# Kernel optimization log

Hardware: AMD Instinct MI355X
Metric: run time of the kernel (lower is better)

The kernel has to match this reference:

```python
import jax, jax.numpy as jnp
import numpy as np
import math

PATCH = 41
NUM_ANG = 8
NUM_SPATIAL = 4
BIN_KSIZE = 2 * int(PATCH / (NUM_SPATIAL + 1))   # 16
BIN_STRIDE = PATCH // NUM_SPATIAL                # 10
BIN_PAD = BIN_KSIZE // 4                         # 4
CLIPVAL = 0.2
EPS = 1e-10
N = 8192


def _sift_pooling_kernel(ksize: int) -> np.ndarray:
    k2 = float(ksize) / 2.0
    xc2 = k2 - np.abs(np.arange(ksize, dtype=np.float32) + 0.5 - k2)
    return (np.outer(xc2, xc2) / k2 ** 2).astype(np.float32)


def _sift_weighting_kernel(ksize: int) -> np.ndarray:
    # Gauss, vlfeat sigma: sigma_mul_2 = ksize**2
    k2 = float(ksize) / 2.0
    ys = np.arange(ksize, dtype=np.float32)[:, None]
    xs = np.arange(ksize, dtype=np.float32)[None, :]
    disq = (ys - k2 + 0.5) ** 2 + (xs - k2 + 0.5) ** 2
    return np.exp(-disq / float(ksize ** 2)).astype(np.float32)


def setup_inputs() -> dict:
    key = jax.random.key(0)
    x = jax.random.normal(key, (N, 1, PATCH, PATCH), dtype=jnp.float32)
    gk = jnp.asarray(_sift_weighting_kernel(PATCH))   # [41,41]
    pk = jnp.asarray(_sift_pooling_kernel(BIN_KSIZE))  # [16,16]
    return {"x": x, "gk": gk, "pk": pk}


def _l2_normalize(v):
    return v / jnp.maximum(jnp.linalg.norm(v, axis=1, keepdims=True), 1e-12)


def reference(x, gk, pk):
    # gradients via replicate-pad + central difference (matches [-1,0,1] convs)
    xp = jnp.pad(x, ((0, 0), (0, 0), (0, 0), (1, 1)), mode='edge')
    gx = xp[..., 2:] - xp[..., :-2]
    yp = jnp.pad(x, ((0, 0), (0, 0), (1, 1), (0, 0)), mode='edge')
    gy = yp[:, :, 2:, :] - yp[:, :, :-2, :]

    mag = jnp.sqrt(gx * gx + gy * gy + EPS) * gk  # gaussian-weighted magnitude
    ori = jnp.arctan2(gy, gx + EPS)

    # soft angular binning
    o_big = (ori + 2.0 * math.pi) / (2.0 * math.pi) * NUM_ANG
    bo0f = jnp.floor(o_big)
    wo1 = o_big - bo0f
    bo0 = bo0f.astype(jnp.int32) % NUM_ANG
    bo1 = (bo0 + 1) % NUM_ANG
    # [N,1,P,P,nb]
    contrib = (jax.nn.one_hot(bo0, NUM_ANG, dtype=mag.dtype) * ((1.0 - wo1) * mag)[..., None]
               + jax.nn.one_hot(bo1, NUM_ANG, dtype=mag.dtype) * (wo1 * mag)[..., None])
    contrib = jnp.transpose(contrib[:, 0], (0, 3, 1, 2))  # [N,nb,P,P]

    # depthwise weighted spatial pooling (same triangular kernel per angular bin)
    kern = jnp.broadcast_to(pk[None, None], (NUM_ANG, 1, BIN_KSIZE, BIN_KSIZE))
    pooled = jax.lax.conv_general_dilated(
        contrib, kern,
        window_strides=(BIN_STRIDE, BIN_STRIDE),
        padding=[(BIN_PAD, BIN_PAD), (BIN_PAD, BIN_PAD)],
        feature_group_count=NUM_ANG,
        dimension_numbers=('NCHW', 'OIHW', 'NCHW'))  # [N,nb,4,4]

    desc = pooled.reshape(pooled.shape[0], -1)  # [N,128]
    desc = _l2_normalize(desc)
    desc = jnp.clip(desc, 0.0, CLIPVAL)
    desc = _l2_normalize(desc)
    # rootsift: sqrt of L1-normalized descriptor
    desc = desc / jnp.maximum(jnp.sum(jnp.abs(desc), axis=1, keepdims=True), 1e-12)
    return jnp.sqrt(desc + 1e-10)
```

## Files before the change

### kernel.cpp

```cpp
#include <hip/hip_runtime.h>
#include <hip/hip_fp16.h>
#include <math.h>

#define PATCH 41
#define PP 1681
#define NB 8
#define STRIDE 10
#define PAD 4
#define NTH 192
#define XR 51
#define HR 5

__device__ __forceinline__ constexpr float tri16(int k) {
    float d = (float)k + 0.5f - 8.0f;
    float a = d < 0.0f ? -d : d;
    return (8.0f - a) * 0.125f;
}

__device__ __forceinline__ uint4 pixel_contrib(float gx, float gy, float w) {
    float X = gx + 1e-10f;
    float mag = __builtin_amdgcn_sqrtf(fmaf(gx, gx, fmaf(gy, gy, 1e-10f))) * w;

    float ax = fabsf(X), ay = fabsf(gy);
    float mx = fmaxf(ax, ay), mn = fminf(ax, ay);
    float r = mn * __builtin_amdgcn_rcpf(fmaxf(mx, 1e-30f));
    float r2 = r * r;
    float a4 = fmaf(r2, -0.0149238f, 0.0670406f);
    a4 = fmaf(r2, a4, -0.1482457f);
    a4 = fmaf(r2, a4, 0.2464287f);
    a4 = fmaf(r2, a4, -0.4235106f);
    a4 = fmaf(r2, a4, 1.2732106f);
    a4 *= r;

    bool sw = ay > ax;
    bool xn = X < 0.0f;
    bool yn = gy < 0.0f;
    int q = (xn ? 2 : 0) + ((sw != xn) ? 1 : 0);
    int b0 = yn ? 7 - q : q;
    bool f = (sw != xn) != yn;
    float ma = a4 * mag;
    float mb = mag - ma;
    float v0 = f ? ma : mb;
    float v1 = f ? mb : ma;

    unsigned combo = __builtin_bit_cast(unsigned, __builtin_amdgcn_cvt_pkrtz(v0, v1));
    int sh = (b0 & 3) << 4;
    unsigned long long A = (unsigned long long)combo << sh;
    unsigned long long B = ((b0 & 3) == 3) ? (unsigned long long)(combo >> 16) : 0ull;
    bool lohalf = b0 < 4;
    unsigned long long lo = lohalf ? A : B;
    unsigned long long hi = lohalf ? B : A;
    uint4 cw;
    cw.x = (unsigned)lo; cw.y = (unsigned)(lo >> 32);
    cw.z = (unsigned)hi; cw.w = (unsigned)(hi >> 32);
    return cw;
}

__global__ __launch_bounds__(NTH, 8) void sift_desc_kernel(
        const float* __restrict__ x,
        const float* __restrict__ gk,
        const float* __restrict__ pk,
        float* __restrict__ out)
{
    const int patch = blockIdx.x;
    const int t = threadIdx.x;

    __shared__ __align__(16) float s_xp[PATCH * XR];
    __shared__ __align__(16) float s_wl[64];
    __shared__ __align__(16) __half s_H[49 * HR * NB];
    __shared__ float s_desc[128];

    const float* xp = x + (size_t)patch * PP;
    {
        int i = t / PATCH;
        int j = t - i * PATCH;
        for (int p = t; p < PP; p += NTH) {
            s_xp[i * XR + j + 6] = xp[p];
            j += 28; i += 4;
            if (j >= PATCH) { j -= PATCH; i += 1; }
        }
    }
    for (int q = t; q < 41 * 9; q += NTH) {
        int i = q / 9;
        int c = q - i * 9;
        int j = (c < 6) ? (c - 6) : (c + 35);
        int jc = min(max(j, 0), PATCH - 1);
        s_xp[i * XR + j + 6] = xp[i * PATCH + jc];
    }
    if (t < 64) {
        int ox = t >> 4, kx = t & 15;
        int col = ox * STRIDE - PAD + kx;
        float d = (float)(col - 20);
        float g = __builtin_amdgcn_exp2f(d * d * -8.582362e-4f);
        bool oob = (col < 0) | (col > PATCH - 1);
        s_wl[t] = oob ? 0.0f : tri16(kx) * g;
    }
    if (t < 160) {
        int dw = (t < 80) ? t : (820 + t);
        ((unsigned*)s_H)[dw] = 0u;
    }
    __syncthreads();

    if (t < PATCH * 4) {
        const int row = t >> 2;
        const int ox = t & 3;
        const int rowM = row * XR + ox * STRIDE + 2;
        const int rowU = (row > 0 ? row - 1 : 0) * XR + ox * STRIDE + 2;
        const int rowD = (row < PATCH - 1 ? row + 1 : PATCH - 1) * XR + ox * STRIDE + 2;

        float drow = (float)(row - 20);
        const float rf = __builtin_amdgcn_exp2f(drow * drow * -8.582362e-4f);

        float wf[16];
        {
            const float4* wl4 = (const float4*)&s_wl[ox << 4];
            float4 w0 = wl4[0], w1 = wl4[1], w2 = wl4[2], w3 = wl4[3];
            wf[0] = w0.x * rf;  wf[1] = w0.y * rf;  wf[2] = w0.z * rf;  wf[3] = w0.w * rf;
            wf[4] = w1.x * rf;  wf[5] = w1.y * rf;  wf[6] = w1.z * rf;  wf[7] = w1.w * rf;
            wf[8] = w2.x * rf;  wf[9] = w2.y * rf;  wf[10] = w2.z * rf; wf[11] = w2.w * rf;
            wf[12] = w3.x * rf; wf[13] = w3.y * rf; wf[14] = w3.z * rf; wf[15] = w3.w * rf;
        }

        float xm1 = s_xp[rowM - 1];
        float x0  = s_xp[rowM];
        float x1  = s_xp[rowM + 1];

        const __half2 z2 = __float2half2_rn(0.0f);
        __half2 a0 = z2, a1 = z2, a2 = z2, a3 = z2;

        #pragma unroll
        for (int it = 0; it < 8; ++it) {
            const int kx0 = 2 * it;
            float x2 = s_xp[rowM + kx0 + 2];
            float x3 = s_xp[rowM + kx0 + 3];
            float u0 = s_xp[rowU + kx0];
            float u1 = s_xp[rowU + kx0 + 1];
            float d0 = s_xp[rowD + kx0];
            float d1 = s_xp[rowD + kx0 + 1];

            uint4 c0 = pixel_contrib(x1 - xm1, d0 - u0, wf[kx0]);
            uint4 c1 = pixel_contrib(x2 - x0,  d1 - u1, wf[kx0 + 1]);

            a0 = __hadd2(a0, __hadd2(*(__half2*)&c0.x, *(__half2*)&c1.x));
            a1 = __hadd2(a1, __hadd2(*(__half2*)&c0.y, *(__half2*)&c1.y));
            a2 = __hadd2(a2, __hadd2(*(__half2*)&c0.z, *(__half2*)&c1.z));
            a3 = __hadd2(a3, __hadd2(*(__half2*)&c0.w, *(__half2*)&c1.w));

            xm1 = x1; x0 = x2; x1 = x3;
        }

        uint4 hv;
        hv.x = *(unsigned*)&a0;
        hv.y = *(unsigned*)&a1;
        hv.z = *(unsigned*)&a2;
        hv.w = *(unsigned*)&a3;
        *(uint4*)&s_H[((row + 4) * HR + ox) * NB] = hv;
    }
    __syncthreads();

    if (t < 128) {
        int b = t >> 4;
        int oy = (t >> 2) & 3;
        int ox = t & 3;
        const __half* hp = &s_H[(oy * STRIDE * HR + ox) * NB + b];
        float v = 0.0f;
        #pragma unroll
        for (int ky = 0; ky < 16; ++ky) {
            v = fmaf(tri16(ky), __half2float(hp[ky * HR * NB]), v);
        }
        s_desc[t] = v;
    }
    __syncthreads();

    if (t < 64) {
        float a = s_desc[t];
        float b = s_desc[t + 64];

        float ss = fmaf(a, a, b * b);
        #pragma unroll
        for (int o = 32; o > 0; o >>= 1) ss += __shfl_xor(ss, o);
        float inv = 1.0f / fmaxf(__builtin_amdgcn_sqrtf(ss), 1e-12f);
        a = fminf(fmaxf(a * inv, 0.0f), 0.2f);
        b = fminf(fmaxf(b * inv, 0.0f), 0.2f);

        float ss2 = fmaf(a, a, b * b);
        #pragma unroll
        for (int o = 32; o > 0; o >>= 1) ss2 += __shfl_xor(ss2, o);
        float inv2 = 1.0f / fmaxf(__builtin_amdgcn_sqrtf(ss2), 1e-12f);
        a *= inv2; b *= inv2;

        float l1 = a + b;
        #pragma unroll
        for (int o = 32; o > 0; o >>= 1) l1 += __shfl_xor(l1, o);
        float invl = 1.0f / fmaxf(l1, 1e-12f);

        float* op = out + (size_t)patch * 128;
        op[t]      = __builtin_amdgcn_sqrtf(fmaf(a, invl, 1e-10f));
        op[t + 64] = __builtin_amdgcn_sqrtf(fmaf(b, invl, 1e-10f));
    }
}

extern "C" void kernel_launch(void* const* d_in, const int* in_sizes, int n_in,
                              void* d_out, int out_size, void* d_ws, size_t ws_size,
                              hipStream_t stream) {
    const float* x  = (const float*)d_in[0];
    const float* gk = (const float*)d_in[1];
    const float* pk = (const float*)d_in[2];
    float* out = (float*)d_out;
    const int n = in_sizes[0] / PP;
    sift_desc_kernel<<<n, NTH, 0, stream>>>(x, gk, pk, out);
}
```

Baseline: 117.1 us.

## Share overlapping horizontal pixel contributions across lanes via DPP instead of recomputing

Each thread now evaluates pixel_contrib for only 11 unique columns of its row segment instead of the full 16-wide pooling window. The overlapping columns owned by neighbouring column threads are pulled in with DPP row shifts and weighted by the triangular kernel in fp16 FMA. This removes the duplicated gradient, orientation and magnitude work caused by the overlapping 16-wide, stride-10 windows. In exchange it adds cross-lane DPP operations and edge masking, and moves the triangular weighting into fp16 arithmetic, which can change rounding.

Result: no change. 115.4 us (-1.5%).

```diff
diff --git a/kernel.cpp b/kernel.cpp
--- a/kernel.cpp
+++ b/kernel.cpp
@@ -56,6 +56,17 @@
     return cw;
 }
 
+__device__ __forceinline__ __half2 u2h2(unsigned v) {
+    return __builtin_bit_cast(__half2, v);
+}
+
+__device__ __forceinline__ unsigned dpp_prev(unsigned v) {
+    return (unsigned)__builtin_amdgcn_update_dpp(0, (int)v, 0x111, 0xF, 0xF, true);
+}
+__device__ __forceinline__ unsigned dpp_next(unsigned v) {
+    return (unsigned)__builtin_amdgcn_update_dpp(0, (int)v, 0x101, 0xF, 0xF, true);
+}
+
 __global__ __launch_bounds__(NTH, 8) void sift_desc_kernel(
         const float* __restrict__ x,
         const float* __restrict__ gk,
@@ -66,7 +77,7 @@
     const int t = threadIdx.x;
 
     __shared__ __align__(16) float s_xp[PATCH * XR];
-    __shared__ __align__(16) float s_wl[64];
+    __shared__ __align__(16) float s_gc[48];
     __shared__ __align__(16) __half s_H[49 * HR * NB];
     __shared__ float s_desc[128];
 
@@ -87,13 +98,10 @@
         int jc = min(max(j, 0), PATCH - 1);
         s_xp[i * XR + j + 6] = xp[i * PATCH + jc];
     }
-    if (t < 64) {
-        int ox = t >> 4, kx = t & 15;
-        int col = ox * STRIDE - PAD + kx;
-        float d = (float)(col - 20);
+    if (t < 48) {
+        float d = (float)(t - 20);
         float g = __builtin_amdgcn_exp2f(d * d * -8.582362e-4f);
-        bool oob = (col < 0) | (col > PATCH - 1);
-        s_wl[t] = oob ? 0.0f : tri16(kx) * g;
+        s_gc[t] = (t < PATCH) ? g : 0.0f;
     }
     if (t < 160) {
         int dw = (t < 80) ? t : (820 + t);
@@ -104,22 +112,13 @@
     if (t < PATCH * 4) {
         const int row = t >> 2;
         const int ox = t & 3;
-        const int rowM = row * XR + ox * STRIDE + 2;
-        const int rowU = (row > 0 ? row - 1 : 0) * XR + ox * STRIDE + 2;
-        const int rowD = (row < PATCH - 1 ? row + 1 : PATCH - 1) * XR + ox * STRIDE + 2;
+        const int cb = ox * STRIDE;
+        const int rowM = row * XR + cb + 6;
+        const int rowU = (row > 0 ? row - 1 : 0) * XR + cb + 6;
+        const int rowD = (row < PATCH - 1 ? row + 1 : PATCH - 1) * XR + cb + 6;
 
         float drow = (float)(row - 20);
         const float rf = __builtin_amdgcn_exp2f(drow * drow * -8.582362e-4f);
-
-        float wf[16];
-        {
-            const float4* wl4 = (const float4*)&s_wl[ox << 4];
-            float4 w0 = wl4[0], w1 = wl4[1], w2 = wl4[2], w3 = wl4[3];
-            wf[0] = w0.x * rf;  wf[1] = w0.y * rf;  wf[2] = w0.z * rf;  wf[3] = w0.w * rf;
-            wf[4] = w1.x * rf;  wf[5] = w1.y * rf;  wf[6] = w1.z * rf;  wf[7] = w1.w * rf;
-            wf[8] = w2.x * rf;  wf[9] = w2.y * rf;  wf[10] = w2.z * rf; wf[11] = w2.w * rf;
-            wf[12] = w3.x * rf; wf[13] = w3.y * rf; wf[14] = w3.z * rf; wf[15] = w3.w * rf;
-        }
 
         float xm1 = s_xp[rowM - 1];
         float x0  = s_xp[rowM];
@@ -128,32 +127,59 @@
         const __half2 z2 = __float2half2_rn(0.0f);
         __half2 a0 = z2, a1 = z2, a2 = z2, a3 = z2;
 
-        #pragma unroll
-        for (int it = 0; it < 8; ++it) {
-            const int kx0 = 2 * it;
-            float x2 = s_xp[rowM + kx0 + 2];
-            float x3 = s_xp[rowM + kx0 + 3];
-            float u0 = s_xp[rowU + kx0];
-            float u1 = s_xp[rowU + kx0 + 1];
-            float d0 = s_xp[rowD + kx0];
-            float d1 = s_xp[rowD + kx0 + 1];
-
-            uint4 c0 = pixel_contrib(x1 - xm1, d0 - u0, wf[kx0]);
-            uint4 c1 = pixel_contrib(x2 - x0,  d1 - u1, wf[kx0 + 1]);
-
-            a0 = __hadd2(a0, __hadd2(*(__half2*)&c0.x, *(__half2*)&c1.x));
-            a1 = __hadd2(a1, __hadd2(*(__half2*)&c0.y, *(__half2*)&c1.y));
-            a2 = __hadd2(a2, __hadd2(*(__half2*)&c0.z, *(__half2*)&c1.z));
-            a3 = __hadd2(a3, __hadd2(*(__half2*)&c0.w, *(__half2*)&c1.w));
-
-            xm1 = x1; x0 = x2; x1 = x3;
+        const bool ox0 = (ox == 0);
+        const bool ox3 = (ox == 3);
+        const __half2 wl[4] = {
+            ox0 ? z2 : __float2half2_rn(tri16(0)),
+            ox0 ? z2 : __float2half2_rn(tri16(1)),
+            ox0 ? z2 : __float2half2_rn(tri16(2)),
+            ox0 ? z2 : __float2half2_rn(tri16(3))
+        };
+
+        #pragma unroll
+        for (int k = 0; k <= 10; ++k) {
+            float x2 = s_xp[rowM + k + 2];
+            float u  = s_xp[rowU + k];
+            float dn = s_xp[rowD + k];
+            float gw = s_gc[cb + k] * rf;
+
+            uint4 cw = pixel_contrib(x1 - xm1, dn - u, gw);
+
+            const __half2 wo = __float2half2_rn(tri16(k + 4));
+            a0 = __hfma2(u2h2(cw.x), wo, a0);
+            a1 = __hfma2(u2h2(cw.y), wo, a1);
+            a2 = __hfma2(u2h2(cw.z), wo, a2);
+            a3 = __hfma2(u2h2(cw.w), wo, a3);
+
+            if (k == 1) {
+                unsigned rx = dpp_next(cw.x);
+                unsigned ry = dpp_next(cw.y);
+                unsigned rz = dpp_next(cw.z);
+                unsigned rw = dpp_next(cw.w);
+                rx = ox3 ? 0u : rx;  ry = ox3 ? 0u : ry;
+                rz = ox3 ? 0u : rz;  rw = ox3 ? 0u : rw;
+                const __half2 wr = __float2half2_rn(tri16(15));
+                a0 = __hfma2(u2h2(rx), wr, a0);
+                a1 = __hfma2(u2h2(ry), wr, a1);
+                a2 = __hfma2(u2h2(rz), wr, a2);
+                a3 = __hfma2(u2h2(rw), wr, a3);
+            }
+            if (k >= 6 && k < 10) {
+                const __half2 wk = wl[k - 6];
+                a0 = __hfma2(u2h2(dpp_prev(cw.x)), wk, a0);
+                a1 = __hfma2(u2h2(dpp_prev(cw.y)), wk, a1);
+                a2 = __hfma2(u2h2(dpp_prev(cw.z)), wk, a2);
+                a3 = __hfma2(u2h2(dpp_prev(cw.w)), wk, a3);
+            }
+
+            xm1 = x0; x0 = x1; x1 = x2;
         }
 
         uint4 hv;
-        hv.x = *(unsigned*)&a0;
-        hv.y = *(unsigned*)&a1;
-        hv.z = *(unsigned*)&a2;
-        hv.w = *(unsigned*)&a3;
+        hv.x = __builtin_bit_cast(unsigned, a0);
+        hv.y = __builtin_bit_cast(unsigned, a1);
+        hv.z = __builtin_bit_cast(unsigned, a2);
+        hv.w = __builtin_bit_cast(unsigned, a3);
         *(uint4*)&s_H[((row + 4) * HR + ox) * NB] = hv;
     }
     __syncthreads();
```
